# Performance work log

Measured on AMD Instinct MI355X. Metric: run time of the kernel, lower is better.

The kernel has to match this reference:

```python
import jax, jax.numpy as jnp
import numpy as np

N = 4096      # num_nodes
U = 64        # num_units
IN = 2        # input_dim
DIM = U + IN  # 66
H = 4         # attention heads
ALPHA = 0.2   # leaky slope inside attention scores
SLOPE = 0.01  # nn.LeakyReLU() default for subnet activations
NEG_INF = -9e15


def setup_inputs() -> dict:
    key = jax.random.key(0)
    ks = jax.random.split(key, 20)
    def gn(k, shape, fan):
        return jax.random.normal(k, shape, dtype=jnp.float32) / np.float32(np.sqrt(fan))
    adj = jax.random.randint(ks[2], (N, N), 0, 2, dtype=jnp.int32)
    adj = jnp.maximum(adj, jnp.eye(N, dtype=jnp.int32))  # ensure self-loops
    return {
        "inputs": jax.random.normal(ks[0], (1, N * IN), dtype=jnp.float32),
        "hx": jax.random.normal(ks[1], (1, N, U), dtype=jnp.float32),
        "adj": adj,
        "m1_W": gn(ks[3], (H, DIM, DIM), DIM),
        "m1_a1": gn(ks[4], (H, DIM), DIM),
        "m1_a2": gn(ks[5], (H, DIM), DIM),
        "m1_Wout": gn(ks[6], (H * DIM, DIM), H * DIM),
        "m1_ao1": gn(ks[7], (DIM,), DIM),
        "m1_ao2": gn(ks[8], (DIM,), DIM),
        "m2_W": gn(ks[9], (H, DIM, DIM), DIM),
        "m2_a1": gn(ks[10], (H, DIM), DIM),
        "m2_a2": gn(ks[11], (H, DIM), DIM),
        "m2_Wout": gn(ks[12], (H * DIM, DIM), H * DIM),
        "m2_ao1": gn(ks[13], (DIM,), DIM),
        "m2_ao2": gn(ks[14], (DIM,), DIM),
        "g1_W": gn(ks[15], (DIM, 2 * U), DIM),
        "g1_b": jnp.zeros((2 * U,), dtype=jnp.float32),
        "g2_W": gn(ks[16], (DIM, U), DIM),
        "g2_b": jnp.zeros((U,), dtype=jnp.float32),
    }


def gat_layer(x, W, a1, a2, mask):
    # x: [N,Fin], W: [Fin,Fout], a1/a2: [Fout], mask: [N,N] bool
    h = x @ W                                   # [N,Fout]
    f1 = h @ a1                                 # [N] source term
    f2 = h @ a2                                 # [N] target term
    e = jax.nn.leaky_relu(f1[:, None] + f2[None, :], ALPHA)  # [N,N]
    e = jnp.where(mask, e, NEG_INF)
    attn = jax.nn.softmax(e, axis=-1)
    return attn @ h                             # [N,Fout]


def subnet(x, W, a1, a2, Wout, ao1, ao2, mask):
    # multi-head GAT, concat heads, activation, output GAT layer, activation
    heads = jax.vmap(gat_layer, in_axes=(None, 0, 0, 0, None))(x, W, a1, a2, mask)  # [H,N,DIM]
    hcat = jnp.transpose(heads, (1, 0, 2)).reshape(x.shape[0], -1)                   # [N,H*DIM]
    hcat = jax.nn.leaky_relu(hcat, SLOPE)
    out = gat_layer(hcat, Wout, ao1, ao2, mask)                                      # [N,DIM]
    return jax.nn.leaky_relu(out, SLOPE)


def reference(inputs, hx, adj, m1_W, m1_a1, m1_a2, m1_Wout, m1_ao1, m1_ao2,
              m2_W, m2_a1, m2_a2, m2_Wout, m2_ao1, m2_ao2,
              g1_W, g1_b, g2_W, g2_b):
    mask = adj > 0
    xi = inputs.reshape(N, IN)
    xh = hx.reshape(N, U)
    # _GAT1: concat(inputs, hx) -> GATSubNet1 -> linear -> sigmoid -> split r,u
    x1 = jnp.concatenate([xi, xh], axis=-1)                 # [N,DIM]
    g1 = subnet(x1, m1_W, m1_a1, m1_a2, m1_Wout, m1_ao1, m1_ao2, mask)
    value = jax.nn.sigmoid(g1 @ g1_W + g1_b)                # [N,2U]
    r, u = value[:, :U], value[:, U:]
    # _GAT2: concat(inputs, r*hx) -> GATSubNet2 -> linear -> tanh
    x2 = jnp.concatenate([xi, r * xh], axis=-1)             # [N,DIM]
    g2 = subnet(x2, m2_W, m2_a1, m2_a2, m2_Wout, m2_ao1, m2_ao2, mask)
    c = jnp.tanh(g2 @ g2_W + g2_b)                          # [N,U]
    new_state = u * xh + (1.0 - u) * c
    return new_state.reshape(1, N, U)
```

## Files before the change

kernel.cpp:

```cpp
#include <hip/hip_runtime.h>
#include <hip/hip_bf16.h>

constexpr int kN = 4096;
constexpr int kDim = 66;
constexpr int kH = 4;
constexpr int kU = 64;
constexpr float kAlpha = 0.2f;
constexpr float kSlope = 0.01f;
constexpr float kLog2e = 1.44269504f;

typedef __attribute__((ext_vector_type(8))) short short8;
typedef __attribute__((ext_vector_type(4))) float floatx4;

__device__ inline unsigned short f2bf(float x){
  unsigned int u = __float_as_uint(x);
  unsigned int r = (u + 0x7FFFu + ((u >> 16) & 1u)) >> 16;
  return (unsigned short)r;
}
__device__ inline float bf2f(unsigned short v){
  return __uint_as_float((unsigned int)v << 16);
}
__device__ inline unsigned int fkey(float f){
  unsigned int u = __float_as_uint(f);
  return (u & 0x80000000u) ? ~u : (u | 0x80000000u);
}
__device__ inline float funkey(unsigned int k){
  unsigned int u = (k & 0x80000000u) ? (k ^ 0x80000000u) : ~k;
  return __uint_as_float(u);
}

__global__ void setup_k(const int* __restrict__ adj, unsigned long long* __restrict__ packed,
                        const float* __restrict__ in2, const float* __restrict__ hx,
                        unsigned short* __restrict__ x1b, unsigned short* __restrict__ x2b,
                        const float* __restrict__ m1W, const float* __restrict__ m1a1, const float* __restrict__ m1a2,
                        const float* __restrict__ m1Wo, const float* __restrict__ m1ao1, const float* __restrict__ m1ao2,
                        const float* __restrict__ m2W, const float* __restrict__ m2a1, const float* __restrict__ m2a2,
                        const float* __restrict__ m2Wo, const float* __restrict__ m2ao1, const float* __restrict__ m2ao2,
                        const float* __restrict__ g1W, const float* __restrict__ g1b,
                        const float* __restrict__ g2W, const float* __restrict__ g2b,
                        unsigned short* __restrict__ B1t, unsigned short* __restrict__ B1t2,
                        unsigned short* __restrict__ B2t, unsigned short* __restrict__ B2t2,
                        unsigned short* __restrict__ Bgt, unsigned short* __restrict__ Bft,
                        unsigned int* __restrict__ fmaxbuf){
  int bb = blockIdx.x, t = threadIdx.x;
  if (bb < 16384){
    int gid = bb * 256 + t;
    unsigned long long m = __ballot(adj[gid] != 0);
    if ((t & 63) == 0) packed[gid >> 6] = m;
    return;
  }
  if (bb < 16384 + 1024){
    int i = (bb - 16384) * 4 + (t >> 6);
    int c = t & 63;
    x1b[(size_t)i * 96 + 2 + c] = f2bf(hx[(size_t)i * kU + c]);
    if (c < 2){
      unsigned short xv = f2bf(in2[i * 2 + c]);
      x1b[(size_t)i * 96 + c] = xv;
      x2b[(size_t)i * 96 + c] = xv;
    }
    return;
  }
  int b = bb - (16384 + 1024);
  if (b < 8){
    int m = b & 3;
    const float* W  = (b < 4 ? m1W  : m2W)  + (size_t)m * kDim * kDim;
    const float* a1 = (b < 4 ? m1a1 : m2a1) + m * kDim;
    const float* a2 = (b < 4 ? m1a2 : m2a2) + m * kDim;
    unsigned short* Bo = (b < 4 ? B1t : B1t2) + (size_t)m * 80 * 96;
    __shared__ float Ws[kDim * kDim];
    __shared__ float wa1s[kDim], wa2s[kDim];
    for (int z = t; z < kDim * kDim; z += 256) Ws[z] = W[z];
    __syncthreads();
    if (t < kDim){
      float s1 = 0.f, s2 = 0.f;
      for (int d = 0; d < kDim; d++){ float wv = Ws[t * kDim + d]; s1 += wv * a1[d]; s2 += wv * a2[d]; }
      wa1s[t] = s1; wa2s[t] = s2;
    }
    __syncthreads();
    for (int z = t; z < 80 * 96; z += 256){
      int nn = z / 96, k = z % 96;
      float val = 0.f;
      if (k < kDim){
        if (nn < kDim) val = Ws[k * kDim + nn];
        else if (nn == 66) val = wa1s[k];
        else if (nn == 67) val = wa2s[k];
      }
      Bo[z] = f2bf(val);
    }
  } else if (b < 10){
    const float* Wo  = (b == 8 ? m1Wo  : m2Wo);
    const float* ao1 = (b == 8 ? m1ao1 : m2ao1);
    const float* ao2 = (b == 8 ? m1ao2 : m2ao2);
    unsigned short* Bo = (b == 8 ? B2t : B2t2);
    __shared__ float wo1s[264], wo2s[264];
    for (int k = t; k < 264; k += 256){
      float s1 = 0.f, s2 = 0.f;
      for (int d = 0; d < kDim; d++){ float wv = Wo[(size_t)k * kDim + d]; s1 += wv * ao1[d]; s2 += wv * ao2[d]; }
      wo1s[k] = s1; wo2s[k] = s2;
    }
    __syncthreads();
    for (int z = t; z < 80 * 288; z += 256){
      int nn = z / 288, k = z % 288;
      float val = 0.f;
      if (k < 264){
        if (nn < kDim) val = Wo[(size_t)k * kDim + nn];
        else if (nn == 66) val = wo1s[k];
        else if (nn == 67) val = wo2s[k];
      }
      Bo[z] = f2bf(val);
    }
  } else if (b == 10){
    for (int z = t; z < 128 * 96; z += 256){
      int nn = z / 96, k = z % 96;
      float val = 0.f;
      if (k < kDim) val = g1W[k * 128 + nn];
      else if (k == 66) val = g1b[nn];
      Bgt[z] = f2bf(val);
    }
  } else {
    if (t < 16) fmaxbuf[t] = 0u;
    for (int z = t; z < 64 * 96; z += 256){
      int nn = z / 96, k = z % 96;
      float val = 0.f;
      if (k < kDim) val = g2W[k * 64 + nn];
      else if (k == 66) val = g2b[nn];
      Bft[z] = f2bf(val);
    }
  }
}

template<int KSTEPS, int NT, int EPI>
__global__ __launch_bounds__(256) void gemm_k(
    const unsigned short* __restrict__ A, const unsigned short* __restrict__ Bt,
    void* __restrict__ p0, void* __restrict__ p1, void* __restrict__ p2,
    const float* __restrict__ aux, unsigned int* __restrict__ fmaxp)
{
  constexpr int KP = KSTEPS * 32;
  const int m = blockIdx.y;
  const int i0 = blockIdx.x * 64;
  const int t = threadIdx.x;
  const int w = t >> 6, lane = t & 63, q = lane >> 4, n = lane & 15;
  const int arow = i0 + w * 16 + n;
  const unsigned short* Ar = A + (size_t)arow * KP;
  const unsigned short* Bm = Bt + (size_t)m * (NT * 16) * KP;
  floatx4 acc[NT];
  #pragma unroll
  for (int v = 0; v < NT; v++) acc[v] = (floatx4){0.f, 0.f, 0.f, 0.f};
  #pragma unroll
  for (int ks = 0; ks < KSTEPS; ks++){
    short8 af = *(const short8*)&Ar[ks * 32 + q * 8];
    #pragma unroll
    for (int nt = 0; nt < NT; nt++){
      short8 bf = *(const short8*)&Bm[(size_t)(nt * 16 + n) * KP + ks * 32 + q * 8];
      acc[nt] = __builtin_amdgcn_mfma_f32_16x16x32_bf16(af, bf, acc[nt], 0, 0, 0);
    }
  }
  const int ib = i0 + w * 16 + q * 4;
  if constexpr (EPI == 0){
    unsigned short* Ht = (unsigned short*)p0 + (size_t)m * 80 * kN;
    float* f1 = (float*)p1 + (size_t)m * kN;
    float* f2 = (float*)p2 + (size_t)m * kN;
    float lm = -3e38f;
    #pragma unroll
    for (int nt = 0; nt < NT; nt++){
      int c = nt * 16 + n;
      if (c < kDim){
        uint2 pk;
        pk.x = ((unsigned)f2bf(acc[nt][1]) << 16) | f2bf(acc[nt][0]);
        pk.y = ((unsigned)f2bf(acc[nt][3]) << 16) | f2bf(acc[nt][2]);
        *(uint2*)&Ht[(size_t)c * kN + ib] = pk;
      } else if (c == 66){
        float4 fv; fv.x = acc[nt][0] * kLog2e; fv.y = acc[nt][1] * kLog2e;
        fv.z = acc[nt][2] * kLog2e; fv.w = acc[nt][3] * kLog2e;
        *(float4*)&f1[ib] = fv;
        *(uint2*)&Ht[(size_t)66 * kN + ib] = make_uint2(0x3F803F80u, 0x3F803F80u);
      } else if (c == 67){
        float4 fv; fv.x = acc[nt][0] * kLog2e; fv.y = acc[nt][1] * kLog2e;
        fv.z = acc[nt][2] * kLog2e; fv.w = acc[nt][3] * kLog2e;
        *(float4*)&f2[ib] = fv;
        lm = fmaxf(fmaxf(fv.x, fv.y), fmaxf(fv.z, fv.w));
        *(uint2*)&Ht[(size_t)67 * kN + ib] = make_uint2(0u, 0u);
      } else {
        *(uint2*)&Ht[(size_t)c * kN + ib] = make_uint2(0u, 0u);
      }
    }
    lm = fmaxf(lm, __shfl_xor(lm, 16));
    lm = fmaxf(lm, __shfl_xor(lm, 32));
    if (lane == 3) atomicMax(&fmaxp[m], fkey(lm));
  } else if constexpr (EPI == 1){
    float* u = (float*)p0;
    unsigned short* x2b = (unsigned short*)p1;
    #pragma unroll
    for (int nt = 0; nt < NT; nt++){
      int c = nt * 16 + n;
      #pragma unroll
      for (int r = 0; r < 4; r++){
        float v = 1.f / (1.f + __expf(-acc[nt][r]));
        if (c < 64) x2b[(size_t)(ib + r) * 96 + 2 + c] = f2bf(v * aux[(size_t)(ib + r) * kU + c]);
        else        u[(size_t)(ib + r) * kU + (c - 64)] = v;
      }
    }
  } else {
    float* outp = (float*)p0;
    const float* u = (const float*)p1;
    #pragma unroll
    for (int nt = 0; nt < NT; nt++){
      int c = nt * 16 + n;
      #pragma unroll
      for (int r = 0; r < 4; r++){
        float cc = tanhf(acc[nt][r]);
        float uv = u[(size_t)(ib + r) * kU + c];
        outp[(size_t)(ib + r) * kU + c] = uv * aux[(size_t)(ib + r) * kU + c] + (1.f - uv) * cc;
      }
    }
  }
}

__global__ __launch_bounds__(256, 4) void attn_mfma_k(
    const unsigned short* __restrict__ Ht, const float* __restrict__ f1,
    const float* __restrict__ f2, const unsigned int* __restrict__ fmaxu,
    const unsigned long long* __restrict__ packed,
    unsigned short* __restrict__ paccb)
{
  const int m = blockIdx.y, js = blockIdx.z;
  const int i0 = blockIdx.x * 64;
  const int t = threadIdx.x;
  const int w = t >> 6, lane = t & 63, q = lane >> 4, n = lane & 15;
  const int i = i0 + w * 16 + n;
  const unsigned short* Hg = Ht + (size_t)m * 80 * kN;
  const float* f2m = f2 + (size_t)m * kN;
  const float f1v = f1[(size_t)m * kN + i];
  const float fmx = funkey(fmaxu[m]);
  const float t0 = f1v + fmx;
  const float S = fmaxf(t0, kAlpha * t0);

  __shared__ __align__(16) unsigned short HtL[80 * 136];
  __shared__ __align__(16) float f2s[128];

  floatx4 acc[5];
  #pragma unroll
  for (int v = 0; v < 5; v++) acc[v] = (floatx4){0.f, 0.f, 0.f, 0.f};

  const int jbase = js * 1024;
  const unsigned long long* prow = packed + (size_t)i * 64;
  for (int ch = 0; ch < 8; ch++){
    const int j0 = jbase + ch * 128;
    __syncthreads();
    for (int z = t; z < 80 * 16; z += 256){
      int row = z >> 4, c16 = z & 15;
      *(uint4*)&HtL[row * 136 + c16 * 8] = *(const uint4*)&Hg[(size_t)row * kN + j0 + c16 * 8];
    }
    if (t < 128) f2s[t] = f2m[j0 + t];
    __syncthreads();
    unsigned long long w0 = prow[(j0 >> 6)];
    unsigned long long w1 = prow[(j0 >> 6) + 1];
    #pragma unroll
    for (int ks = 0; ks < 4; ks++){
      unsigned long long wsel = (ks < 2) ? w0 : w1;
      unsigned int bits = (unsigned int)((wsel >> ((ks & 1) * 32 + q * 8)) & 0xffull);
      float4 fa = *(const float4*)&f2s[ks * 32 + q * 8];
      float4 fb = *(const float4*)&f2s[ks * 32 + q * 8 + 4];
      float fv[8] = {fa.x, fa.y, fa.z, fa.w, fb.x, fb.y, fb.z, fb.w};
      float p[8];
      #pragma unroll
      for (int e = 0; e < 8; e++){
        float tt = f1v + fv[e];
        float ee = fmaxf(tt, kAlpha * tt);
        float pv = __builtin_amdgcn_exp2f(ee - S);
        p[e] = ((bits >> e) & 1u) ? pv : 0.f;
      }
      union { short8 s; unsigned int u[4]; } af;
      #pragma unroll
      for (int e2 = 0; e2 < 4; e2++)
        af.u[e2] = __builtin_amdgcn_perm(__float_as_uint(p[2 * e2 + 1]), __float_as_uint(p[2 * e2]), 0x07060302u);
      #pragma unroll
      for (int nt = 0; nt < 5; nt++){
        const short8 bf = *(const short8*)&HtL[(nt * 16 + n) * 136 + ks * 32 + q * 8];
        acc[nt] = __builtin_amdgcn_mfma_f32_16x16x32_bf16(af.s, bf, acc[nt], 0, 0, 0);
      }
    }
  }
  unsigned short* pw = paccb + ((size_t)(m * 4 + js) * kN + (i0 + w * 16)) * 80;
  #pragma unroll
  for (int nt = 0; nt < 5; nt++){
    #pragma unroll
    for (int r = 0; r < 4; r++)
      pw[(q * 4 + r) * 80 + nt * 16 + n] = f2bf(acc[nt][r]);
  }
}

__global__ void combine_k(const unsigned short* __restrict__ paccb, unsigned short* __restrict__ outb,
                          int ostride, int ones_col){
  int m = blockIdx.y;
  int i = blockIdx.x * 64 + (threadIdx.x >> 2);
  int cg = threadIdx.x & 3;
  const unsigned short* p0 = paccb + ((size_t)(m * 4) * kN + i) * 80;
  const unsigned short* p1 = p0 + (size_t)kN * 80;
  const unsigned short* p2 = p1 + (size_t)kN * 80;
  const unsigned short* p3 = p2 + (size_t)kN * 80;
  float l = bf2f(p0[66]) + bf2f(p1[66]) + bf2f(p2[66]) + bf2f(p3[66]);
  float inv = 1.f / l;
  unsigned short* orow = outb + (size_t)i * ostride + m * kDim;
  #pragma unroll
  for (int cc = 0; cc < 17; cc++){
    int c = cg * 17 + cc;
    if (c < kDim){
      float v = (bf2f(p0[c]) + bf2f(p1[c]) + bf2f(p2[c]) + bf2f(p3[c])) * inv;
      v = fmaxf(v, kSlope * v);
      orow[c] = f2bf(v);
    }
  }
  if (ones_col && cg == 3) orow[66] = 0x3F80;
}

extern "C" void kernel_launch(void* const* d_in, const int* in_sizes, int n_in,
                              void* d_out, int out_size, void* d_ws, size_t ws_size,
                              hipStream_t stream){
  const float* inputs  = (const float*)d_in[0];
  const float* hx      = (const float*)d_in[1];
  const int*   adj     = (const int*)d_in[2];
  const float* m1_W    = (const float*)d_in[3];
  const float* m1_a1   = (const float*)d_in[4];
  const float* m1_a2   = (const float*)d_in[5];
  const float* m1_Wout = (const float*)d_in[6];
  const float* m1_ao1  = (const float*)d_in[7];
  const float* m1_ao2  = (const float*)d_in[8];
  const float* m2_W    = (const float*)d_in[9];
  const float* m2_a1   = (const float*)d_in[10];
  const float* m2_a2   = (const float*)d_in[11];
  const float* m2_Wout = (const float*)d_in[12];
  const float* m2_ao1  = (const float*)d_in[13];
  const float* m2_ao2  = (const float*)d_in[14];
  const float* g1_W    = (const float*)d_in[15];
  const float* g1_b    = (const float*)d_in[16];
  const float* g2_W    = (const float*)d_in[17];
  const float* g2_b    = (const float*)d_in[18];
  float* out = (float*)d_out;

  char* ws = (char*)d_ws;
  size_t off = 0;
  auto alloc = [&](size_t bytes) -> void* {
    void* p = ws + off;
    off = (off + bytes + 255) & ~(size_t)255;
    return p;
  };
  unsigned long long* packed = (unsigned long long*)alloc((size_t)kN * 64 * 8);
  unsigned short* x1b  = (unsigned short*)alloc((size_t)kN * 96 * 2);
  unsigned short* x2b  = (unsigned short*)alloc((size_t)kN * 96 * 2);
  unsigned short* Ht   = (unsigned short*)alloc((size_t)kH * 80 * kN * 2);
  unsigned short* Hto  = (unsigned short*)alloc((size_t)80 * kN * 2);
  unsigned short* hcatb= (unsigned short*)alloc((size_t)kN * 288 * 2);
  unsigned short* gb   = (unsigned short*)alloc((size_t)kN * 96 * 2);
  unsigned short* g2b  = (unsigned short*)alloc((size_t)kN * 96 * 2);
  float* f1   = (float*)alloc((size_t)kH * kN * 4);
  float* f2   = (float*)alloc((size_t)kH * kN * 4);
  float* fo1  = (float*)alloc((size_t)kN * 4);
  float* fo2  = (float*)alloc((size_t)kN * 4);
  unsigned int* fmaxbuf = (unsigned int*)alloc(64);
  float* u    = (float*)alloc((size_t)kN * kU * 4);
  unsigned short* paccb = (unsigned short*)alloc((size_t)16 * kN * 80 * 2);
  unsigned short* B1t  = (unsigned short*)alloc((size_t)kH * 80 * 96 * 2);
  unsigned short* B1t2 = (unsigned short*)alloc((size_t)kH * 80 * 96 * 2);
  unsigned short* B2t  = (unsigned short*)alloc((size_t)80 * 288 * 2);
  unsigned short* B2t2 = (unsigned short*)alloc((size_t)80 * 288 * 2);
  unsigned short* Bgt  = (unsigned short*)alloc((size_t)128 * 96 * 2);
  unsigned short* Bft  = (unsigned short*)alloc((size_t)64 * 96 * 2);
  (void)ws_size; (void)in_sizes; (void)n_in; (void)out_size;

  setup_k<<<16384 + 1024 + 12, 256, 0, stream>>>(adj, packed, inputs, hx, x1b, x2b,
      m1_W, m1_a1, m1_a2, m1_Wout, m1_ao1, m1_ao2,
      m2_W, m2_a1, m2_a2, m2_Wout, m2_ao1, m2_ao2,
      g1_W, g1_b, g2_W, g2_b,
      B1t, B1t2, B2t, B2t2, Bgt, Bft, fmaxbuf);

  gemm_k<3, 5, 0><<<dim3(64, kH), 256, 0, stream>>>(x1b, B1t, Ht, f1, f2, nullptr, fmaxbuf + 0);
  attn_mfma_k<<<dim3(64, kH, 4), 256, 0, stream>>>(Ht, f1, f2, fmaxbuf + 0, packed, paccb);
  combine_k<<<dim3(64, kH), 256, 0, stream>>>(paccb, hcatb, 288, 0);
  gemm_k<9, 5, 0><<<dim3(64, 1), 256, 0, stream>>>(hcatb, B2t, Hto, fo1, fo2, nullptr, fmaxbuf + 4);
  attn_mfma_k<<<dim3(64, 1, 4), 256, 0, stream>>>(Hto, fo1, fo2, fmaxbuf + 4, packed, paccb);
  combine_k<<<dim3(64, 1), 256, 0, stream>>>(paccb, gb, 96, 1);
  gemm_k<3, 8, 1><<<dim3(64, 1), 256, 0, stream>>>(gb, Bgt, u, x2b, nullptr, hx, nullptr);

  gemm_k<3, 5, 0><<<dim3(64, kH), 256, 0, stream>>>(x2b, B1t2, Ht, f1, f2, nullptr, fmaxbuf + 5);
  attn_mfma_k<<<dim3(64, kH, 4), 256, 0, stream>>>(Ht, f1, f2, fmaxbuf + 5, packed, paccb);
  combine_k<<<dim3(64, kH), 256, 0, stream>>>(paccb, hcatb, 288, 0);
  gemm_k<9, 5, 0><<<dim3(64, 1), 256, 0, stream>>>(hcatb, B2t2, Hto, fo1, fo2, nullptr, fmaxbuf + 9);
  attn_mfma_k<<<dim3(64, 1, 4), 256, 0, stream>>>(Hto, fo1, fo2, fmaxbuf + 9, packed, paccb);
  combine_k<<<dim3(64, 1), 256, 0, stream>>>(paccb, g2b, 96, 1);
  gemm_k<3, 4, 2><<<dim3(64, 1), 256, 0, stream>>>(g2b, Bft, out, u, nullptr, hx, nullptr);
}
```

Baseline: 349.3 us.

## Factor attention exponentials into per-row/per-column fp16 products and use fp16 MFMA

Switches all intermediate storage and MFMA from bf16 to fp16. The leaky-relu exponential is factored into separable terms: exp2(max(t, αt) - S) becomes the max of two products, each a per-row scale times a per-column value. The per-column values are precomputed once per chunk in shared memory, which replaces eight exp2 calls per element with packed half2 multiplies and a max. It also shrinks the H^T buffer from 80 to 68 rows, zero-fills the padding in LDS, and doubles the j-split for the output-layer attention to 8 for more parallelism. The fp16 range and precision of the factored exponentials may cause overflow or accuracy loss for extreme scores.

```diff
diff --git a/kernel.cpp b/kernel.cpp
--- a/kernel.cpp
+++ b/kernel.cpp
@@ -9,17 +9,10 @@
 constexpr float kSlope = 0.01f;
 constexpr float kLog2e = 1.44269504f;
 
-typedef __attribute__((ext_vector_type(8))) short short8;
+typedef _Float16 half8 __attribute__((ext_vector_type(8)));
+typedef _Float16 half2t __attribute__((ext_vector_type(2)));
 typedef __attribute__((ext_vector_type(4))) float floatx4;
 
-__device__ inline unsigned short f2bf(float x){
-  unsigned int u = __float_as_uint(x);
-  unsigned int r = (u + 0x7FFFu + ((u >> 16) & 1u)) >> 16;
-  return (unsigned short)r;
-}
-__device__ inline float bf2f(unsigned short v){
-  return __uint_as_float((unsigned int)v << 16);
-}
 __device__ inline unsigned int fkey(float f){
   unsigned int u = __float_as_uint(f);
   return (u & 0x80000000u) ? ~u : (u | 0x80000000u);
@@ -31,16 +24,16 @@
 
 __global__ void setup_k(const int* __restrict__ adj, unsigned long long* __restrict__ packed,
                         const float* __restrict__ in2, const float* __restrict__ hx,
-                        unsigned short* __restrict__ x1b, unsigned short* __restrict__ x2b,
+                        _Float16* __restrict__ x1b, _Float16* __restrict__ x2b,
                         const float* __restrict__ m1W, const float* __restrict__ m1a1, const float* __restrict__ m1a2,
                         const float* __restrict__ m1Wo, const float* __restrict__ m1ao1, const float* __restrict__ m1ao2,
                         const float* __restrict__ m2W, const float* __restrict__ m2a1, const float* __restrict__ m2a2,
                         const float* __restrict__ m2Wo, const float* __restrict__ m2ao1, const float* __restrict__ m2ao2,
                         const float* __restrict__ g1W, const float* __restrict__ g1b,
                         const float* __restrict__ g2W, const float* __restrict__ g2b,
-                        unsigned short* __restrict__ B1t, unsigned short* __restrict__ B1t2,
-                        unsigned short* __restrict__ B2t, unsigned short* __restrict__ B2t2,
-                        unsigned short* __restrict__ Bgt, unsigned short* __restrict__ Bft,
+                        _Float16* __restrict__ B1t, _Float16* __restrict__ B1t2,
+                        _Float16* __restrict__ B2t, _Float16* __restrict__ B2t2,
+                        _Float16* __restrict__ Bgt, _Float16* __restrict__ Bft,
                         unsigned int* __restrict__ fmaxbuf){
   int bb = blockIdx.x, t = threadIdx.x;
   if (bb < 16384){
@@ -52,11 +45,15 @@
   if (bb < 16384 + 1024){
     int i = (bb - 16384) * 4 + (t >> 6);
     int c = t & 63;
-    x1b[(size_t)i * 96 + 2 + c] = f2bf(hx[(size_t)i * kU + c]);
+    x1b[(size_t)i * 96 + 2 + c] = (_Float16)hx[(size_t)i * kU + c];
     if (c < 2){
-      unsigned short xv = f2bf(in2[i * 2 + c]);
+      _Float16 xv = (_Float16)in2[i * 2 + c];
       x1b[(size_t)i * 96 + c] = xv;
       x2b[(size_t)i * 96 + c] = xv;
+    }
+    if (c < 30){
+      x1b[(size_t)i * 96 + 66 + c] = (_Float16)0.f;
+      x2b[(size_t)i * 96 + 66 + c] = (_Float16)0.f;
     }
     return;
   }
@@ -66,7 +63,7 @@
     const float* W  = (b < 4 ? m1W  : m2W)  + (size_t)m * kDim * kDim;
     const float* a1 = (b < 4 ? m1a1 : m2a1) + m * kDim;
     const float* a2 = (b < 4 ? m1a2 : m2a2) + m * kDim;
-    unsigned short* Bo = (b < 4 ? B1t : B1t2) + (size_t)m * 80 * 96;
+    _Float16* Bo = (b < 4 ? B1t : B1t2) + (size_t)m * 80 * 96;
     __shared__ float Ws[kDim * kDim];
     __shared__ float wa1s[kDim], wa2s[kDim];
     for (int z = t; z < kDim * kDim; z += 256) Ws[z] = W[z];
@@ -85,13 +82,13 @@
         else if (nn == 66) val = wa1s[k];
         else if (nn == 67) val = wa2s[k];
       }
-      Bo[z] = f2bf(val);
+      Bo[z] = (_Float16)val;
     }
   } else if (b < 10){
     const float* Wo  = (b == 8 ? m1Wo  : m2Wo);
     const float* ao1 = (b == 8 ? m1ao1 : m2ao1);
     const float* ao2 = (b == 8 ? m1ao2 : m2ao2);
-    unsigned short* Bo = (b == 8 ? B2t : B2t2);
+    _Float16* Bo = (b == 8 ? B2t : B2t2);
     __shared__ float wo1s[264], wo2s[264];
     for (int k = t; k < 264; k += 256){
       float s1 = 0.f, s2 = 0.f;
@@ -107,7 +104,7 @@
         else if (nn == 66) val = wo1s[k];
         else if (nn == 67) val = wo2s[k];
       }
-      Bo[z] = f2bf(val);
+      Bo[z] = (_Float16)val;
     }
   } else if (b == 10){
     for (int z = t; z < 128 * 96; z += 256){
@@ -115,7 +112,7 @@
       float val = 0.f;
       if (k < kDim) val = g1W[k * 128 + nn];
       else if (k == 66) val = g1b[nn];
-      Bgt[z] = f2bf(val);
+      Bgt[z] = (_Float16)val;
     }
   } else {
     if (t < 16) fmaxbuf[t] = 0u;
@@ -124,14 +121,14 @@
       float val = 0.f;
       if (k < kDim) val = g2W[k * 64 + nn];
       else if (k == 66) val = g2b[nn];
-      Bft[z] = f2bf(val);
+      Bft[z] = (_Float16)val;
     }
   }
 }
 
 template<int KSTEPS, int NT, int EPI>
 __global__ __launch_bounds__(256) void gemm_k(
-    const unsigned short* __restrict__ A, const unsigned short* __restrict__ Bt,
+    const _Float16* __restrict__ A, const _Float16* __restrict__ Bt,
     void* __restrict__ p0, void* __restrict__ p1, void* __restrict__ p2,
     const float* __restrict__ aux, unsigned int* __restrict__ fmaxp)
 {
@@ -141,23 +138,23 @@
   const int t = threadIdx.x;
   const int w = t >> 6, lane = t & 63, q = lane >> 4, n = lane & 15;
   const int arow = i0 + w * 16 + n;
-  const unsigned short* Ar = A + (size_t)arow * KP;
-  const unsigned short* Bm = Bt + (size_t)m * (NT * 16) * KP;
+  const _Float16* Ar = A + (size_t)arow * KP;
+  const _Float16* Bm = Bt + (size_t)m * (NT * 16) * KP;
   floatx4 acc[NT];
   #pragma unroll
   for (int v = 0; v < NT; v++) acc[v] = (floatx4){0.f, 0.f, 0.f, 0.f};
   #pragma unroll
   for (int ks = 0; ks < KSTEPS; ks++){
-    short8 af = *(const short8*)&Ar[ks * 32 + q * 8];
+    half8 af = *(const half8*)&Ar[ks * 32 + q * 8];
     #pragma unroll
     for (int nt = 0; nt < NT; nt++){
-      short8 bf = *(const short8*)&Bm[(size_t)(nt * 16 + n) * KP + ks * 32 + q * 8];
-      acc[nt] = __builtin_amdgcn_mfma_f32_16x16x32_bf16(af, bf, acc[nt], 0, 0, 0);
+      half8 bf = *(const half8*)&Bm[(size_t)(nt * 16 + n) * KP + ks * 32 + q * 8];
+      acc[nt] = __builtin_amdgcn_mfma_f32_16x16x32_f16(af, bf, acc[nt], 0, 0, 0);
     }
   }
   const int ib = i0 + w * 16 + q * 4;
   if constexpr (EPI == 0){
-    unsigned short* Ht = (unsigned short*)p0 + (size_t)m * 80 * kN;
+    _Float16* Ht = (_Float16*)p0 + (size_t)m * 68 * kN;
     float* f1 = (float*)p1 + (size_t)m * kN;
     float* f2 = (float*)p2 + (size_t)m * kN;
     float lm = -3e38f;
@@ -165,23 +162,21 @@
     for (int nt = 0; nt < NT; nt++){
       int c = nt * 16 + n;
       if (c < kDim){
-        uint2 pk;
-        pk.x = ((unsigned)f2bf(acc[nt][1]) << 16) | f2bf(acc[nt][0]);
-        pk.y = ((unsigned)f2bf(acc[nt][3]) << 16) | f2bf(acc[nt][2]);
-        *(uint2*)&Ht[(size_t)c * kN + ib] = pk;
+        union { _Float16 h[4]; uint2 v; } pk;
+        pk.h[0] = (_Float16)acc[nt][0]; pk.h[1] = (_Float16)acc[nt][1];
+        pk.h[2] = (_Float16)acc[nt][2]; pk.h[3] = (_Float16)acc[nt][3];
+        *(uint2*)&Ht[(size_t)c * kN + ib] = pk.v;
       } else if (c == 66){
         float4 fv; fv.x = acc[nt][0] * kLog2e; fv.y = acc[nt][1] * kLog2e;
         fv.z = acc[nt][2] * kLog2e; fv.w = acc[nt][3] * kLog2e;
         *(float4*)&f1[ib] = fv;
-        *(uint2*)&Ht[(size_t)66 * kN + ib] = make_uint2(0x3F803F80u, 0x3F803F80u);
+        *(uint2*)&Ht[(size_t)66 * kN + ib] = make_uint2(0x3C003C00u, 0x3C003C00u);
       } else if (c == 67){
         float4 fv; fv.x = acc[nt][0] * kLog2e; fv.y = acc[nt][1] * kLog2e;
         fv.z = acc[nt][2] * kLog2e; fv.w = acc[nt][3] * kLog2e;
         *(float4*)&f2[ib] = fv;
         lm = fmaxf(fmaxf(fv.x, fv.y), fmaxf(fv.z, fv.w));
         *(uint2*)&Ht[(size_t)67 * kN + ib] = make_uint2(0u, 0u);
-      } else {
-        *(uint2*)&Ht[(size_t)c * kN + ib] = make_uint2(0u, 0u);
       }
     }
     lm = fmaxf(lm, __shfl_xor(lm, 16));
@@ -189,14 +184,14 @@
     if (lane == 3) atomicMax(&fmaxp[m], fkey(lm));
   } else if constexpr (EPI == 1){
     float* u = (float*)p0;
-    unsigned short* x2b = (unsigned short*)p1;
+    _Float16* x2b = (_Float16*)p1;
     #pragma unroll
     for (int nt = 0; nt < NT; nt++){
       int c = nt * 16 + n;
       #pragma unroll
       for (int r = 0; r < 4; r++){
         float v = 1.f / (1.f + __expf(-acc[nt][r]));
-        if (c < 64) x2b[(size_t)(ib + r) * 96 + 2 + c] = f2bf(v * aux[(size_t)(ib + r) * kU + c]);
+        if (c < 64) x2b[(size_t)(ib + r) * 96 + 2 + c] = (_Float16)(v * aux[(size_t)(ib + r) * kU + c]);
         else        u[(size_t)(ib + r) * kU + (c - 64)] = v;
       }
     }
@@ -216,41 +211,54 @@
   }
 }
 
+template<int JSPLIT>
 __global__ __launch_bounds__(256, 4) void attn_mfma_k(
-    const unsigned short* __restrict__ Ht, const float* __restrict__ f1,
+    const _Float16* __restrict__ Ht, const float* __restrict__ f1,
     const float* __restrict__ f2, const unsigned int* __restrict__ fmaxu,
     const unsigned long long* __restrict__ packed,
-    unsigned short* __restrict__ paccb)
+    _Float16* __restrict__ paccb)
 {
+  constexpr int JR = kN / JSPLIT;
+  constexpr int NCH = JR / 128;
   const int m = blockIdx.y, js = blockIdx.z;
   const int i0 = blockIdx.x * 64;
   const int t = threadIdx.x;
   const int w = t >> 6, lane = t & 63, q = lane >> 4, n = lane & 15;
   const int i = i0 + w * 16 + n;
-  const unsigned short* Hg = Ht + (size_t)m * 80 * kN;
+  const _Float16* Hg = Ht + (size_t)m * 68 * kN;
   const float* f2m = f2 + (size_t)m * kN;
   const float f1v = f1[(size_t)m * kN + i];
   const float fmx = funkey(fmaxu[m]);
   const float t0 = f1v + fmx;
   const float S = fmaxf(t0, kAlpha * t0);
-
-  __shared__ __align__(16) unsigned short HtL[80 * 136];
-  __shared__ __align__(16) float f2s[128];
+  const float A1f = __builtin_amdgcn_exp2f(t0 - S);
+  const float A2f = __builtin_amdgcn_exp2f(kAlpha * t0 - S);
+  const half2t a1p = { (_Float16)A1f, (_Float16)A1f };
+  const half2t a2p = { (_Float16)A2f, (_Float16)A2f };
+
+  __shared__ __align__(16) _Float16 HtL[80 * 136];
+  __shared__ __align__(16) _Float16 B1h[128], B2h[128];
+
+  for (int z = t; z < 12 * 136; z += 256) HtL[68 * 136 + z] = (_Float16)0.f;
 
   floatx4 acc[5];
   #pragma unroll
   for (int v = 0; v < 5; v++) acc[v] = (floatx4){0.f, 0.f, 0.f, 0.f};
 
-  const int jbase = js * 1024;
+  const int jbase = js * JR;
   const unsigned long long* prow = packed + (size_t)i * 64;
-  for (int ch = 0; ch < 8; ch++){
+  for (int ch = 0; ch < NCH; ch++){
     const int j0 = jbase + ch * 128;
     __syncthreads();
-    for (int z = t; z < 80 * 16; z += 256){
+    for (int z = t; z < 68 * 16; z += 256){
       int row = z >> 4, c16 = z & 15;
       *(uint4*)&HtL[row * 136 + c16 * 8] = *(const uint4*)&Hg[(size_t)row * kN + j0 + c16 * 8];
     }
-    if (t < 128) f2s[t] = f2m[j0 + t];
+    if (t < 128){
+      float v = f2m[j0 + t] - fmx;
+      B1h[t] = (_Float16)__builtin_amdgcn_exp2f(v);
+      B2h[t] = (_Float16)__builtin_amdgcn_exp2f(kAlpha * v);
+    }
     __syncthreads();
     unsigned long long w0 = prow[(j0 >> 6)];
     unsigned long long w1 = prow[(j0 >> 6) + 1];
@@ -258,59 +266,67 @@
     for (int ks = 0; ks < 4; ks++){
       unsigned long long wsel = (ks < 2) ? w0 : w1;
       unsigned int bits = (unsigned int)((wsel >> ((ks & 1) * 32 + q * 8)) & 0xffull);
-      float4 fa = *(const float4*)&f2s[ks * 32 + q * 8];
-      float4 fb = *(const float4*)&f2s[ks * 32 + q * 8 + 4];
-      float fv[8] = {fa.x, fa.y, fa.z, fa.w, fb.x, fb.y, fb.z, fb.w};
-      float p[8];
-      #pragma unroll
-      for (int e = 0; e < 8; e++){
-        float tt = f1v + fv[e];
-        float ee = fmaxf(tt, kAlpha * tt);
-        float pv = __builtin_amdgcn_exp2f(ee - S);
-        p[e] = ((bits >> e) & 1u) ? pv : 0.f;
-      }
-      union { short8 s; unsigned int u[4]; } af;
-      #pragma unroll
-      for (int e2 = 0; e2 < 4; e2++)
-        af.u[e2] = __builtin_amdgcn_perm(__float_as_uint(p[2 * e2 + 1]), __float_as_uint(p[2 * e2]), 0x07060302u);
+      union { uint4 v; unsigned int u[4]; } b1v, b2v;
+      b1v.v = *(const uint4*)&B1h[ks * 32 + q * 8];
+      b2v.v = *(const uint4*)&B2h[ks * 32 + q * 8];
+      union { half8 s; unsigned int u[4]; } af;
+      #pragma unroll
+      for (int e = 0; e < 4; e++){
+        half2t x1 = __builtin_bit_cast(half2t, b1v.u[e]);
+        half2t x2 = __builtin_bit_cast(half2t, b2v.u[e]);
+        half2t m1 = x1 * a1p;
+        half2t m2 = x2 * a2p;
+        half2t pm = __builtin_elementwise_max(m1, m2);
+        unsigned int mm = (((bits >> (2 * e)) & 1u) ? 0x0000FFFFu : 0u)
+                        | (((bits >> (2 * e + 1)) & 1u) ? 0xFFFF0000u : 0u);
+        af.u[e] = __builtin_bit_cast(unsigned int, pm) & mm;
+      }
       #pragma unroll
       for (int nt = 0; nt < 5; nt++){
-        const short8 bf = *(const short8*)&HtL[(nt * 16 + n) * 136 + ks * 32 + q * 8];
-        acc[nt] = __builtin_amdgcn_mfma_f32_16x16x32_bf16(af.s, bf, acc[nt], 0, 0, 0);
-      }
-    }
-  }
-  unsigned short* pw = paccb + ((size_t)(m * 4 + js) * kN + (i0 + w * 16)) * 80;
+        const half8 bf = *(const half8*)&HtL[(nt * 16 + n) * 136 + ks * 32 + q * 8];
+        acc[nt] = __builtin_amdgcn_mfma_f32_16x16x32_f16(af.s, bf, acc[nt], 0, 0, 0);
+      }
+    }
+  }
+  _Float16* pw = paccb + ((size_t)(m * JSPLIT + js) * kN + (i0 + w * 16)) * 80;
   #pragma unroll
   for (int nt = 0; nt < 5; nt++){
-    #pragma unroll
-    for (int r = 0; r < 4; r++)
-      pw[(q * 4 + r) * 80 + nt * 16 + n] = f2bf(acc[nt][r]);
-  }
-}
-
-__global__ void combine_k(const unsigned short* __restrict__ paccb, unsigned short* __restrict__ outb,
+    if (nt < 4 || n < 4){
+      #pragma unroll
+      for (int r = 0; r < 4; r++)
+        pw[(q * 4 + r) * 80 + nt * 16 + n] = (_Float16)acc[nt][r];
+    }
+  }
+}
+
+template<int JSPLIT>
+__global__ void combine_k(const _Float16* __restrict__ paccb, _Float16* __restrict__ outb,
                           int ostride, int ones_col){
   int m = blockIdx.y;
   int i = blockIdx.x * 64 + (threadIdx.x >> 2);
   int cg = threadIdx.x & 3;
-  const unsigned short* p0 = paccb + ((size_t)(m * 4) * kN + i) * 80;
-  const unsigned short* p1 = p0 + (size_t)kN * 80;
-  const unsigned short* p2 = p1 + (size_t)kN * 80;
-  const unsigned short* p3 = p2 + (size_t)kN * 80;
-  float l = bf2f(p0[66]) + bf2f(p1[66]) + bf2f(p2[66]) + bf2f(p3[66]);
+  const _Float16* ps[JSPLIT];
+  #pragma unroll
+  for (int s = 0; s < JSPLIT; s++)
+    ps[s] = paccb + ((size_t)(m * JSPLIT + s) * kN + i) * 80;
+  float l = 0.f;
+  #pragma unroll
+  for (int s = 0; s < JSPLIT; s++) l += (float)ps[s][66];
   float inv = 1.f / l;
-  unsigned short* orow = outb + (size_t)i * ostride + m * kDim;
+  _Float16* orow = outb + (size_t)i * ostride + m * kDim;
   #pragma unroll
   for (int cc = 0; cc < 17; cc++){
     int c = cg * 17 + cc;
     if (c < kDim){
-      float v = (bf2f(p0[c]) + bf2f(p1[c]) + bf2f(p2[c]) + bf2f(p3[c])) * inv;
+      float v = 0.f;
+      #pragma unroll
+      for (int s = 0; s < JSPLIT; s++) v += (float)ps[s][c];
+      v *= inv;
       v = fmaxf(v, kSlope * v);
-      orow[c] = f2bf(v);
-    }
-  }
-  if (ones_col && cg == 3) orow[66] = 0x3F80;
+      orow[c] = (_Float16)v;
+    }
+  }
+  if (ones_col && cg == 3) orow[66] = (_Float16)1.f;
 }
 
 extern "C" void kernel_launch(void* const* d_in, const int* in_sizes, int n_in,
@@ -345,26 +361,26 @@
     return p;
   };
   unsigned long long* packed = (unsigned long long*)alloc((size_t)kN * 64 * 8);
-  unsigned short* x1b  = (unsigned short*)alloc((size_t)kN * 96 * 2);
-  unsigned short* x2b  = (unsigned short*)alloc((size_t)kN * 96 * 2);
-  unsigned short* Ht   = (unsigned short*)alloc((size_t)kH * 80 * kN * 2);
-  unsigned short* Hto  = (unsigned short*)alloc((size_t)80 * kN * 2);
-  unsigned short* hcatb= (unsigned short*)alloc((size_t)kN * 288 * 2);
-  unsigned short* gb   = (unsigned short*)alloc((size_t)kN * 96 * 2);
-  unsigned short* g2b  = (unsigned short*)alloc((size_t)kN * 96 * 2);
+  _Float16* x1b  = (_Float16*)alloc((size_t)kN * 96 * 2);
+  _Float16* x2b  = (_Float16*)alloc((size_t)kN * 96 * 2);
+  _Float16* Ht   = (_Float16*)alloc((size_t)kH * 68 * kN * 2);
+  _Float16* Hto  = (_Float16*)alloc((size_t)68 * kN * 2);
+  _Float16* hcatb= (_Float16*)alloc((size_t)kN * 288 * 2);
+  _Float16* gb   = (_Float16*)alloc((size_t)kN * 96 * 2);
+  _Float16* g2bv = (_Float16*)alloc((size_t)kN * 96 * 2);
   float* f1   = (float*)alloc((size_t)kH * kN * 4);
   float* f2   = (float*)alloc((size_t)kH * kN * 4);
   float* fo1  = (float*)alloc((size_t)kN * 4);
   float* fo2  = (float*)alloc((size_t)kN * 4);
   unsigned int* fmaxbuf = (unsigned int*)alloc(64);
   float* u    = (float*)alloc((size_t)kN * kU * 4);
-  unsigned short* paccb = (unsigned short*)alloc((size_t)16 * kN * 80 * 2);
-  unsigned short* B1t  = (unsigned short*)alloc((size_t)kH * 80 * 96 * 2);
-  unsigned short* B1t2 = (unsigned short*)alloc((size_t)kH * 80 * 96 * 2);
-  unsigned short* B2t  = (unsigned short*)alloc((size_t)80 * 288 * 2);
-  unsigned short* B2t2 = (unsigned short*)alloc((size_t)80 * 288 * 2);
-  unsigned short* Bgt  = (unsigned short*)alloc((size_t)128 * 96 * 2);
-  unsigned short* Bft  = (unsigned short*)alloc((size_t)64 * 96 * 2);
+  _Float16* paccb = (_Float16*)alloc((size_t)16 * kN * 80 * 2);
+  _Float16* B1t  = (_Float16*)alloc((size_t)kH * 80 * 96 * 2);
+  _Float16* B1t2 = (_Float16*)alloc((size_t)kH * 80 * 96 * 2);
+  _Float16* B2t  = (_Float16*)alloc((size_t)80 * 288 * 2);
+  _Float16* B2t2 = (_Float16*)alloc((size_t)80 * 288 * 2);
+  _Float16* Bgt  = (_Float16*)alloc((size_t)128 * 96 * 2);
+  _Float16* Bft  = (_Float16*)alloc((size_t)64 * 96 * 2);
   (void)ws_size; (void)in_sizes; (void)n_in; (void)out_size;
 
   setup_k<<<16384 + 1024 + 12, 256, 0, stream>>>(adj, packed, inputs, hx, x1b, x2b,
@@ -374,18 +390,18 @@
       B1t, B1t2, B2t, B2t2, Bgt, Bft, fmaxbuf);
 
   gemm_k<3, 5, 0><<<dim3(64, kH), 256, 0, stream>>>(x1b, B1t, Ht, f1, f2, nullptr, fmaxbuf + 0);
-  attn_mfma_k<<<dim3(64, kH, 4), 256, 0, stream>>>(Ht, f1, f2, fmaxbuf + 0, packed, paccb);
-  combine_k<<<dim3(64, kH), 256, 0, stream>>>(paccb, hcatb, 288, 0);
+  attn_mfma_k<4><<<dim3(64, kH, 4), 256, 0, stream>>>(Ht, f1, f2, fmaxbuf + 0, packed, paccb);
+  combine_k<4><<<dim3(64, kH), 256, 0, stream>>>(paccb, hcatb, 288, 0);
   gemm_k<9, 5, 0><<<dim3(64, 1), 256, 0, stream>>>(hcatb, B2t, Hto, fo1, fo2, nullptr, fmaxbuf + 4);
-  attn_mfma_k<<<dim3(64, 1, 4), 256, 0, stream>>>(Hto, fo1, fo2, fmaxbuf + 4, packed, paccb);
-  combine_k<<<dim3(64, 1), 256, 0, stream>>>(paccb, gb, 96, 1);
+  attn_mfma_k<8><<<dim3(64, 1, 8), 256, 0, stream>>>(Hto, fo1, fo2, fmaxbuf + 4, packed, paccb);
+  combine_k<8><<<dim3(64, 1), 256, 0, stream>>>(paccb, gb, 96, 1);
   gemm_k<3, 8, 1><<<dim3(64, 1), 256, 0, stream>>>(gb, Bgt, u, x2b, nullptr, hx, nullptr);
 
   gemm_k<3, 5, 0><<<dim3(64, kH), 256, 0, stream>>>(x2b, B1t2, Ht, f1, f2, nullptr, fmaxbuf + 5);
-  attn_mfma_k<<<dim3(64, kH, 4), 256, 0, stream>>>(Ht, f1, f2, fmaxbuf + 5, packed, paccb);
-  combine_k<<<dim3(64, kH), 256, 0, stream>>>(paccb, hcatb, 288, 0);
+  attn_mfma_k<4><<<dim3(64, kH, 4), 256, 0, stream>>>(Ht, f1, f2, fmaxbuf + 5, packed, paccb);
+  combine_k<4><<<dim3(64, kH), 256, 0, stream>>>(paccb, hcatb, 288, 0);
   gemm_k<9, 5, 0><<<dim3(64, 1), 256, 0, stream>>>(hcatb, B2t2, Hto, fo1, fo2, nullptr, fmaxbuf + 9);
-  attn_mfma_k<<<dim3(64, 1, 4), 256, 0, stream>>>(Hto, fo1, fo2, fmaxbuf + 9, packed, paccb);
-  combine_k<<<dim3(64, 1), 256, 0, stream>>>(paccb, g2b, 96, 1);
-  gemm_k<3, 4, 2><<<dim3(64, 1), 256, 0, stream>>>(g2b, Bft, out, u, nullptr, hx, nullptr);
-}
+  attn_mfma_k<8><<<dim3(64, 1, 8), 256, 0, stream>>>(Hto, fo1, fo2, fmaxbuf + 9, packed, paccb);
+  combine_k<8><<<dim3(64, 1), 256, 0, stream>>>(paccb, g2bv, 96, 1);
+  gemm_k<3, 4, 2><<<dim3(64, 1), 256, 0, stream>>>(g2bv, Bft, out, u, nullptr, hx, nullptr);
+}
```

New measurement: 321.3 us. 1.09x faster.
